# Optimization experiments

Hardware: AMD Instinct MI355X
Metric: run time of the kernel (lower is better)

The kernel has to match this reference:

```python
import jax, jax.numpy as jnp
import numpy as np

N_SRC = 100_000   # hetero[s].num_nodes
N_DST = 100_000   # hetero[d].num_nodes
E     = 800_000   # edge_index.size(1)
D_SRC = 256       # node_dims['src']
D_DST = 256       # node_dims['dst']
D_REL = 128       # d_rel


def setup_inputs() -> dict:
    key = jax.random.key(0)
    ks = jax.random.split(key, 6)
    x_src = jax.random.normal(ks[0], (N_SRC, D_SRC), jnp.float32)
    x_dst = jax.random.normal(ks[1], (N_DST, D_DST), jnp.float32)
    # nn.Linear(d_in, d_rel, bias=False) weights, stored transposed as [d_in, d_rel]
    W_src = jax.random.normal(ks[2], (D_SRC, D_REL), jnp.float32) / np.sqrt(D_SRC).astype(np.float32)
    W_dst = jax.random.normal(ks[3], (D_DST, D_REL), jnp.float32) / np.sqrt(D_DST).astype(np.float32)
    edge_src = jax.random.randint(ks[4], (E,), 0, N_SRC, jnp.int32)  # edge_index[0]
    edge_dst = jax.random.randint(ks[5], (E,), 0, N_DST, jnp.int32)  # edge_index[1]
    return {"x_src": x_src, "x_dst": x_dst, "W_src": W_src, "W_dst": W_dst,
            "edge_src": edge_src, "edge_dst": edge_dst}


def reference(x_src, x_dst, W_src, W_dst, edge_src, edge_dst):
    # Per-type linear projection (bias-free), as in self.proj[nt](feats)
    p_src = x_src @ W_src            # [N_src, d_rel]
    p_dst = x_dst @ W_dst            # projected per module, unused by this edge type
    del p_dst

    # Degree of each destination (A.sum(dim=1)), clamped to >= 1.
    deg = jax.ops.segment_sum(jnp.ones((E,), jnp.float32), edge_dst,
                              num_segments=N_DST)
    deg = jnp.maximum(deg, 1.0)      # [N_dst]

    # Degree-normalized SpMM: sum of source features per destination / deg.
    # (coalescing duplicate edges sums their unit values; segment_sum matches.)
    agg = jax.ops.segment_sum(p_src[edge_src], edge_dst,
                              num_segments=N_DST)            # [N_dst, d_rel]
    dst = agg / deg[:, None]

    # rel_embs[et] = {'dst': dst, 'src_in': x_proj[s], 'deg_dst': deg}
    return dst, p_src, deg
```

## Files before the change

kernel.cpp:

```cpp
#include <hip/hip_runtime.h>
#include <hip/hip_bf16.h>

#define D_SRC 256
#define D_REL 128

typedef __bf16 bf16x8 __attribute__((ext_vector_type(8)));
typedef float f32x4 __attribute__((ext_vector_type(4)));

typedef const __attribute__((address_space(1))) void GASV;
typedef __attribute__((address_space(3))) void LASV;

__global__ void zero_kernel(int* __restrict__ p, int n) {
    int i = blockIdx.x * 256 + threadIdx.x;
    if (i < n) p[i] = 0;
}

__global__ __launch_bounds__(64) void prep_w_kernel(const float* __restrict__ W,
                                                    bf16x8* __restrict__ Wt) {
    int c = blockIdx.x;
    int ks = c >> 3, n = c & 7;
    int lane = threadIdx.x;
    int col = n * 16 + (lane & 15);
    int k0 = ks * 32 + (lane >> 4) * 8;
    bf16x8 v;
#pragma unroll
    for (int j = 0; j < 8; ++j) v[j] = (__bf16)W[(size_t)(k0 + j) * D_REL + col];
    Wt[c * 64 + lane] = v;
}

__global__ __launch_bounds__(256, 4) void proj_mfma_kernel(
    const float* __restrict__ x, const f32x4* __restrict__ Wt,
    float* __restrict__ out, unsigned short* __restrict__ out_bf, int M) {
    __shared__ float xlds[32 * 256];
    int tid = threadIdx.x;
    int wid = tid >> 6, lane = tid & 63;
    int r = lane & 15, kq = lane >> 4;
    int row0 = blockIdx.x * 32;

#pragma unroll
    for (int j = 0; j < 8; ++j) {
        int rl = wid * 8 + j;
        int grow = min(row0 + rl, M - 1);
        const float* src = x + (size_t)grow * D_SRC + ((lane ^ j) << 2);
        __builtin_amdgcn_global_load_lds((GASV*)src, (LASV*)&xlds[rl * 256], 16, 0, 0);
    }

    f32x4 wfv[2][8];
#pragma unroll
    for (int s = 0; s < 2; ++s)
#pragma unroll
        for (int ks = 0; ks < 8; ++ks)
            wfv[s][ks] = Wt[(ks * 8 + wid * 2 + s) * 64 + lane];
#pragma unroll
    for (int s = 0; s < 2; ++s)
#pragma unroll
        for (int ks = 0; ks < 8; ++ks)
            asm volatile("" : "+v"(wfv[s][ks]));

    __syncthreads();

    f32x4 acc[2][2];
#pragma unroll
    for (int t = 0; t < 2; ++t)
#pragma unroll
        for (int s = 0; s < 2; ++s) acc[t][s] = (f32x4)(0.f);

    const f32x4* xl = (const f32x4*)xlds;
    int r8 = r & 7;
#pragma unroll
    for (int ks = 0; ks < 8; ++ks) {
        int q0 = ks * 8 + kq * 2;
#pragma unroll
        for (int t = 0; t < 2; ++t) {
            int rl = t * 16 + r;
            f32x4 a0 = xl[rl * 64 + (q0 ^ r8)];
            f32x4 a1 = xl[rl * 64 + ((q0 + 1) ^ r8)];
            bf16x8 xf;
            xf[0] = (__bf16)a0[0]; xf[1] = (__bf16)a0[1];
            xf[2] = (__bf16)a0[2]; xf[3] = (__bf16)a0[3];
            xf[4] = (__bf16)a1[0]; xf[5] = (__bf16)a1[1];
            xf[6] = (__bf16)a1[2]; xf[7] = (__bf16)a1[3];
            acc[t][0] = __builtin_amdgcn_mfma_f32_16x16x32_bf16(
                __builtin_bit_cast(bf16x8, wfv[0][ks]), xf, acc[t][0], 0, 0, 0);
            acc[t][1] = __builtin_amdgcn_mfma_f32_16x16x32_bf16(
                __builtin_bit_cast(bf16x8, wfv[1][ks]), xf, acc[t][1], 0, 0, 0);
        }
    }

    int col0 = wid * 32;
#pragma unroll
    for (int t = 0; t < 2; ++t) {
        int prow = row0 + t * 16 + r;
        if (prow < M) {
            size_t o0 = (size_t)prow * D_REL + col0 + kq * 4;
            *(f32x4*)(out + o0) = acc[t][0];
            *(f32x4*)(out + o0 + 16) = acc[t][1];
            ushort4 b0, b1;
            b0.x = __bfloat16_as_ushort(__float2bfloat16(acc[t][0][0]));
            b0.y = __bfloat16_as_ushort(__float2bfloat16(acc[t][0][1]));
            b0.z = __bfloat16_as_ushort(__float2bfloat16(acc[t][0][2]));
            b0.w = __bfloat16_as_ushort(__float2bfloat16(acc[t][0][3]));
            b1.x = __bfloat16_as_ushort(__float2bfloat16(acc[t][1][0]));
            b1.y = __bfloat16_as_ushort(__float2bfloat16(acc[t][1][1]));
            b1.z = __bfloat16_as_ushort(__float2bfloat16(acc[t][1][2]));
            b1.w = __bfloat16_as_ushort(__float2bfloat16(acc[t][1][3]));
            *(ushort4*)(out_bf + o0) = b0;
            *(ushort4*)(out_bf + o0 + 16) = b1;
        }
    }
}

__global__ void count_kernel(const int* __restrict__ edge_dst, int* __restrict__ deg_i,
                             int* __restrict__ pos_arr, int E) {
    int e = blockIdx.x * 256 + threadIdx.x;
    if (e < E) pos_arr[e] = atomicAdd(&deg_i[edge_dst[e]], 1);
}

__global__ __launch_bounds__(1024) void scan_blocks(
    const int* __restrict__ deg_i, int* __restrict__ incl,
    int* __restrict__ bsums, int n) {
    int i = blockIdx.x * 1024 + threadIdx.x;
    int v = (i < n) ? deg_i[i] : 0;
    int lane = threadIdx.x & 63;
    int wid = threadIdx.x >> 6;
    int x = v;
#pragma unroll
    for (int off = 1; off < 64; off <<= 1) {
        int y = __shfl_up(x, off, 64);
        if (lane >= off) x += y;
    }
    __shared__ int wsum[16];
    if (lane == 63) wsum[wid] = x;
    __syncthreads();
    if (wid == 0 && lane < 16) {
        int s = wsum[lane];
#pragma unroll
        for (int off = 1; off < 16; off <<= 1) {
            int y = __shfl_up(s, off, 64);
            if (lane >= off) s += y;
        }
        wsum[lane] = s;
    }
    __syncthreads();
    int add = (wid > 0) ? wsum[wid - 1] : 0;
    x += add;
    if (i < n) incl[i] = x;
    if (threadIdx.x == 1023) bsums[blockIdx.x] = x;
}

__global__ __launch_bounds__(128) void scan_sums(int* __restrict__ bs, int nb) {
    __shared__ int tmp[128];
    int t = threadIdx.x;
    int v = (t < nb) ? bs[t] : 0;
    tmp[t] = v;
    __syncthreads();
    for (int off = 1; off < 128; off <<= 1) {
        int y = 0;
        if (t >= off) y = tmp[t - off];
        __syncthreads();
        tmp[t] += y;
        __syncthreads();
    }
    if (t < nb) bs[t] = tmp[t] - v;
}

__global__ __launch_bounds__(1024) void finalize_kernel(
    const int* __restrict__ deg_i, const int* __restrict__ incl,
    const int* __restrict__ bsums, int* __restrict__ row_start,
    float* __restrict__ deg_out, int n, int E) {
    int i = blockIdx.x * 1024 + threadIdx.x;
    if (i < n) {
        int off = bsums[blockIdx.x];
        row_start[i] = off + incl[i] - deg_i[i];
        deg_out[i] = (float)max(deg_i[i], 1);
    }
    if (i == 0) row_start[n] = E;
}

__global__ void fill_kernel(const int* __restrict__ edge_src,
                            const int* __restrict__ edge_dst,
                            const int* __restrict__ row_start,
                            const int* __restrict__ pos_arr,
                            int* __restrict__ bucket, int E) {
    int e = blockIdx.x * 256 + threadIdx.x;
    if (e < E) {
        int d = edge_dst[e];
        bucket[row_start[d] + pos_arr[e]] = edge_src[e];
    }
}

__global__ __launch_bounds__(256) void gather_kernel(
    const unsigned int* __restrict__ p_bf, const int* __restrict__ row_start,
    const int* __restrict__ bucket, const float* __restrict__ deg_out,
    float* __restrict__ dst, int n) {
    int row = blockIdx.x * 4 + (threadIdx.x >> 6);
    int lane = threadIdx.x & 63;
    if (row >= n) return;
    int beg = row_start[row], end = row_start[row + 1];
    float ax = 0.f, ay = 0.f;
    int idx = beg;
    for (; idx + 4 <= end; idx += 4) {
        int s0 = bucket[idx + 0];
        int s1 = bucket[idx + 1];
        int s2 = bucket[idx + 2];
        int s3 = bucket[idx + 3];
        unsigned int v0 = p_bf[(size_t)s0 * 64 + lane];
        unsigned int v1 = p_bf[(size_t)s1 * 64 + lane];
        unsigned int v2 = p_bf[(size_t)s2 * 64 + lane];
        unsigned int v3 = p_bf[(size_t)s3 * 64 + lane];
        ax += __uint_as_float(v0 << 16) + __uint_as_float(v1 << 16)
            + __uint_as_float(v2 << 16) + __uint_as_float(v3 << 16);
        ay += __uint_as_float(v0 & 0xffff0000u) + __uint_as_float(v1 & 0xffff0000u)
            + __uint_as_float(v2 & 0xffff0000u) + __uint_as_float(v3 & 0xffff0000u);
    }
    for (; idx < end; ++idx) {
        int s = bucket[idx];
        unsigned int v = p_bf[(size_t)s * 64 + lane];
        ax += __uint_as_float(v << 16);
        ay += __uint_as_float(v & 0xffff0000u);
    }
    float dinv = 1.0f / deg_out[row];
    float2 o;
    o.x = ax * dinv;
    o.y = ay * dinv;
    ((float2*)dst)[(size_t)row * 64 + lane] = o;
}

extern "C" void kernel_launch(void* const* d_in, const int* in_sizes, int n_in,
                              void* d_out, int out_size, void* d_ws, size_t ws_size,
                              hipStream_t stream) {
    const float* x_src = (const float*)d_in[0];
    const float* W_src = (const float*)d_in[2];
    const int* edge_src = (const int*)d_in[4];
    const int* edge_dst = (const int*)d_in[5];

    const int N_SRC = in_sizes[0] / D_SRC;
    const int N_DST = in_sizes[1] / D_SRC;
    const int E = in_sizes[4];

    float* out_dst = (float*)d_out;
    float* out_psrc = out_dst + (size_t)N_DST * D_REL;
    float* out_deg = out_psrc + (size_t)N_SRC * D_REL;

    int* deg_i = (int*)d_ws;
    int* incl = deg_i + N_DST;
    int* row_start = incl + N_DST;
    int* bsums = row_start + N_DST + 1;
    int* pos_arr = bsums + 128;
    int* bucket = pos_arr + E;
    size_t int_bytes = (size_t)(3 * N_DST + 1 + 128 + 2 * (size_t)E) * sizeof(int);
    size_t wt_off = (int_bytes + 255) & ~(size_t)255;
    bf16x8* Wt = (bf16x8*)((char*)d_ws + wt_off);
    size_t pbf_off = wt_off + 65536;
    unsigned short* p_bf = (unsigned short*)((char*)d_ws + pbf_off);

    zero_kernel<<<(N_DST + 255) / 256, 256, 0, stream>>>(deg_i, N_DST);
    prep_w_kernel<<<64, 64, 0, stream>>>(W_src, Wt);
    proj_mfma_kernel<<<(N_SRC + 31) / 32, 256, 0, stream>>>(
        x_src, (const f32x4*)Wt, out_psrc, p_bf, N_SRC);
    count_kernel<<<(E + 255) / 256, 256, 0, stream>>>(edge_dst, deg_i, pos_arr, E);
    int nb = (N_DST + 1023) / 1024;
    scan_blocks<<<nb, 1024, 0, stream>>>(deg_i, incl, bsums, N_DST);
    scan_sums<<<1, 128, 0, stream>>>(bsums, nb);
    finalize_kernel<<<nb, 1024, 0, stream>>>(deg_i, incl, bsums, row_start, out_deg, N_DST, E);
    fill_kernel<<<(E + 255) / 256, 256, 0, stream>>>(edge_src, edge_dst, row_start, pos_arr, bucket, E);
    gather_kernel<<<(N_DST + 3) / 4, 256, 0, stream>>>(
        (const unsigned int*)p_bf, row_start, bucket, out_deg, out_dst, N_DST);
}
```

Baseline: 146.5 us.

## Split fp32 projection output into separate convert pass, unroll gather, nontemporal stores

The GEMM kernel now writes only the bf16 projection, and a new convert kernel expands bf16 to fp32 for the p_src output using nontemporal stores. The gather loop is unrolled to 8 edges for more memory-level parallelism and uses a nontemporal store for the output. The zero kernel is replaced with hipMemsetAsync. The fp32 p_src output is now bf16-rounded instead of the full fp32 accumulator, which loses precision and adds an extra kernel pass that reads the bf16 buffer back.

```diff
diff --git a/kernel.cpp b/kernel.cpp
--- a/kernel.cpp
+++ b/kernel.cpp
@@ -6,14 +6,10 @@
 
 typedef __bf16 bf16x8 __attribute__((ext_vector_type(8)));
 typedef float f32x4 __attribute__((ext_vector_type(4)));
+typedef float f32x2 __attribute__((ext_vector_type(2)));
 
 typedef const __attribute__((address_space(1))) void GASV;
 typedef __attribute__((address_space(3))) void LASV;
-
-__global__ void zero_kernel(int* __restrict__ p, int n) {
-    int i = blockIdx.x * 256 + threadIdx.x;
-    if (i < n) p[i] = 0;
-}
 
 __global__ __launch_bounds__(64) void prep_w_kernel(const float* __restrict__ W,
                                                     bf16x8* __restrict__ Wt) {
@@ -28,9 +24,9 @@
     Wt[c * 64 + lane] = v;
 }
 
-__global__ __launch_bounds__(256, 4) void proj_mfma_kernel(
+__global__ __launch_bounds__(256, 4) void proj_gemm_kernel(
     const float* __restrict__ x, const f32x4* __restrict__ Wt,
-    float* __restrict__ out, unsigned short* __restrict__ out_bf, int M) {
+    unsigned short* __restrict__ out_bf, int M) {
     __shared__ float xlds[32 * 256];
     int tid = threadIdx.x;
     int wid = tid >> 6, lane = tid & 63;
@@ -93,8 +89,6 @@
         int prow = row0 + t * 16 + r;
         if (prow < M) {
             size_t o0 = (size_t)prow * D_REL + col0 + kq * 4;
-            *(f32x4*)(out + o0) = acc[t][0];
-            *(f32x4*)(out + o0 + 16) = acc[t][1];
             ushort4 b0, b1;
             b0.x = __bfloat16_as_ushort(__float2bfloat16(acc[t][0][0]));
             b0.y = __bfloat16_as_ushort(__float2bfloat16(acc[t][0][1]));
@@ -110,6 +104,25 @@
     }
 }
 
+__global__ __launch_bounds__(256) void convert_kernel(
+    const uint4* __restrict__ p_bf, float* __restrict__ out, int n8) {
+    int i = blockIdx.x * 256 + threadIdx.x;
+    if (i >= n8) return;
+    uint4 v = p_bf[i];
+    f32x4 lo, hi;
+    lo[0] = __uint_as_float(v.x << 16);
+    lo[1] = __uint_as_float(v.x & 0xffff0000u);
+    lo[2] = __uint_as_float(v.y << 16);
+    lo[3] = __uint_as_float(v.y & 0xffff0000u);
+    hi[0] = __uint_as_float(v.z << 16);
+    hi[1] = __uint_as_float(v.z & 0xffff0000u);
+    hi[2] = __uint_as_float(v.w << 16);
+    hi[3] = __uint_as_float(v.w & 0xffff0000u);
+    f32x4* o = (f32x4*)(out + (size_t)i * 8);
+    __builtin_nontemporal_store(lo, o);
+    __builtin_nontemporal_store(hi, o + 1);
+}
+
 __global__ void count_kernel(const int* __restrict__ edge_dst, int* __restrict__ deg_i,
                              int* __restrict__ pos_arr, int E) {
     int e = blockIdx.x * 256 + threadIdx.x;
@@ -199,11 +212,22 @@
     int beg = row_start[row], end = row_start[row + 1];
     float ax = 0.f, ay = 0.f;
     int idx = beg;
+    for (; idx + 8 <= end; idx += 8) {
+        int s[8];
+        unsigned int v[8];
+#pragma unroll
+        for (int u = 0; u < 8; ++u) s[u] = bucket[idx + u];
+#pragma unroll
+        for (int u = 0; u < 8; ++u) v[u] = p_bf[(size_t)s[u] * 64 + lane];
+#pragma unroll
+        for (int u = 0; u < 8; ++u) {
+            ax += __uint_as_float(v[u] << 16);
+            ay += __uint_as_float(v[u] & 0xffff0000u);
+        }
+    }
     for (; idx + 4 <= end; idx += 4) {
-        int s0 = bucket[idx + 0];
-        int s1 = bucket[idx + 1];
-        int s2 = bucket[idx + 2];
-        int s3 = bucket[idx + 3];
+        int s0 = bucket[idx + 0], s1 = bucket[idx + 1];
+        int s2 = bucket[idx + 2], s3 = bucket[idx + 3];
         unsigned int v0 = p_bf[(size_t)s0 * 64 + lane];
         unsigned int v1 = p_bf[(size_t)s1 * 64 + lane];
         unsigned int v2 = p_bf[(size_t)s2 * 64 + lane];
@@ -220,10 +244,11 @@
         ay += __uint_as_float(v & 0xffff0000u);
     }
     float dinv = 1.0f / deg_out[row];
-    float2 o;
-    o.x = ax * dinv;
-    o.y = ay * dinv;
-    ((float2*)dst)[(size_t)row * 64 + lane] = o;
+    f32x2 o;
+    o[0] = ax * dinv;
+    o[1] = ay * dinv;
+    f32x2* dp = (f32x2*)dst + (size_t)row * 64 + lane;
+    __builtin_nontemporal_store(o, dp);
 }
 
 extern "C" void kernel_launch(void* const* d_in, const int* in_sizes, int n_in,
@@ -254,10 +279,15 @@
     size_t pbf_off = wt_off + 65536;
     unsigned short* p_bf = (unsigned short*)((char*)d_ws + pbf_off);
 
-    zero_kernel<<<(N_DST + 255) / 256, 256, 0, stream>>>(deg_i, N_DST);
+    (void)hipMemsetAsync(deg_i, 0, (size_t)N_DST * sizeof(int), stream);
     prep_w_kernel<<<64, 64, 0, stream>>>(W_src, Wt);
-    proj_mfma_kernel<<<(N_SRC + 31) / 32, 256, 0, stream>>>(
-        x_src, (const f32x4*)Wt, out_psrc, p_bf, N_SRC);
+    proj_gemm_kernel<<<(N_SRC + 31) / 32, 256, 0, stream>>>(
+        x_src, (const f32x4*)Wt, p_bf, N_SRC);
+    {
+        int n8 = N_SRC * D_REL / 8;
+        convert_kernel<<<(n8 + 255) / 256, 256, 0, stream>>>(
+            (const uint4*)p_bf, out_psrc, n8);
+    }
     count_kernel<<<(E + 255) / 256, 256, 0, stream>>>(edge_dst, deg_i, pos_arr, E);
     int nb = (N_DST + 1023) / 1024;
     scan_blocks<<<nb, 1024, 0, stream>>>(deg_i, incl, bsums, N_DST);
```

Result: slower. 151.0 us (+3.1%).
